# Kernel optimization log

Measured on AMD Instinct MI355X. Metric: run time of the kernel, lower is better.

Reference implementation:

```python
import jax, jax.numpy as jnp
import numpy as np

IOU_TR = 0.3
SCORE_TR = 0.1
EPS = 1e-9
N_DET = 4096
N_CLASSES = 20


def setup_inputs() -> dict:
    key = jax.random.key(0)
    k1, k2, k3, k4 = jax.random.split(key, 4)
    scores = jax.random.uniform(k1, (N_DET,), dtype=jnp.float32)
    classes = jax.random.randint(k2, (N_DET,), 0, N_CLASSES).astype(jnp.float32)
    centers = jax.random.uniform(k3, (N_DET, 3), dtype=jnp.float32) * 64.0
    dims = jax.random.uniform(k4, (N_DET, 3), dtype=jnp.float32) * 8.0 + 1.0
    results = jnp.concatenate([scores[:, None], classes[:, None], centers, dims], axis=1)
    return {"results": results}


def _pairwise_iou3d(boxes):
    # boxes: [N, 6] = (cx, cy, cz, w, h, d) center format
    c = boxes[:, :3]
    d = boxes[:, 3:]
    lo = c - d * 0.5  # [N,3]
    hi = c + d * 0.5
    inter_lo = jnp.maximum(lo[:, None, :], lo[None, :, :])  # [N,N,3]
    inter_hi = jnp.minimum(hi[:, None, :], hi[None, :, :])
    inter = jnp.prod(jnp.clip(inter_hi - inter_lo, 0.0, None), axis=-1)  # [N,N]
    vol = jnp.prod(d, axis=-1)  # [N]
    union = vol[:, None] + vol[None, :] - inter
    return inter / (union + EPS)


def reference(results):
    # results: [N, 8] = (score, class, cx, cy, cz, w, h, d)
    N = results.shape[0]
    order = jnp.argsort(-results[:, 0])  # sort by score descending
    r = results[order]
    valid = r[:, 0] >= SCORE_TR  # score threshold filter
    iou = _pairwise_iou3d(r[:, 2:])  # [N,N]
    idx = jnp.arange(N)

    def body(i, state):
        keep, active = state
        cur = active[i]
        keep = keep.at[i].set(cur)
        # suppress later boxes whose IoU with box i exceeds threshold
        sup = cur & (iou[i] > IOU_TR) & (idx > i)
        active = active & (~sup)
        return keep, active

    keep, _ = jax.lax.fori_loop(0, N, body, (jnp.zeros(N, dtype=bool), valid))
    # static-shape output: suppressed / filtered rows zeroed instead of compacted
    return jnp.where(keep[:, None], r, jnp.zeros_like(r))
```

## Files before the change

kernel.cpp:

```cpp
#include <hip/hip_runtime.h>

typedef unsigned long long u64;
typedef unsigned int u32;
typedef unsigned short u16;

#define N_DET 4096
#define NW 64
#define IOU_TR 0.3f
#define SCORE_TR 0.1f
#define EPS 1e-9f


__device__ __forceinline__ u64 rl64(u64 v, int l) {
    unsigned lo = __builtin_amdgcn_readlane((unsigned)v, l);
    unsigned hi = __builtin_amdgcn_readlane((unsigned)(v >> 32), l);
    return ((u64)hi << 32) | lo;
}

__global__ void __launch_bounds__(256) k_sort(const float* __restrict__ res,
                                              float* __restrict__ rows,
                                              float* __restrict__ ssc,
                                              float4* __restrict__ soaLO,
                                              float4* __restrict__ soaHI,
                                              u64* __restrict__ A,
                                              u64* __restrict__ Trm) {
    __shared__ float s[N_DET];
    int tid = threadIdx.x;
    if (blockIdx.x == 0) {
        if (tid < 64) A[tid] = 0ull;
        if (tid >= 64 && tid < 128)
            Trm[(size_t)4095 * NW + (tid - 64)] = 0ull;
    }
    for (int j = tid; j < N_DET; j += 256) s[j] = res[j * 8];
    __syncthreads();
    int r = tid >> 4, c = tid & 15;
    int gi = blockIdx.x * 16 + r;
    float sc = s[gi];
    int part = 0;
    int j0 = c * 256;
    for (int j = j0; j < j0 + 256; ++j) {
        float sj = s[j];
        part += (sj > sc) || (sj == sc && j < gi);
    }
    part += __shfl_xor(part, 1, 64);
    part += __shfl_xor(part, 2, 64);
    part += __shfl_xor(part, 4, 64);
    part += __shfl_xor(part, 8, 64);
    if (c == 0) {
        int rank = part;
        float4 a = *(const float4*)(res + gi * 8);
        float4 b = *(const float4*)(res + gi * 8 + 4);
        *(float4*)(rows + rank * 8)     = a;
        *(float4*)(rows + rank * 8 + 4) = b;
        ssc[rank] = a.x;
        float cx = a.z, cy = a.w, cz = b.x, dx = b.y, dy = b.z, dz = b.w;
        soaLO[rank] = make_float4(cx - dx * 0.5f, cy - dy * 0.5f,
                                  cz - dz * 0.5f, (dx * dy) * dz);
        soaHI[rank] = make_float4(cx + dx * 0.5f, cy + dy * 0.5f,
                                  cz + dz * 0.5f, 0.0f);
    }
}

__global__ void __launch_bounds__(256) k_sup(const float4* __restrict__ soaLO,
                                             const float4* __restrict__ soaHI,
                                             const float* __restrict__ ssc,
                                             u64* __restrict__ Trm,
                                             u64* __restrict__ A) {
    __shared__ float s_b[2][7][4][64];
    const int tid = threadIdx.x;
    const int wv = tid >> 6;
    const int lane = tid & 63;
    const int i0 = blockIdx.x * 4;
    const int i = i0 + wv;
    const int w0 = i0 >> 6;
    const bool valid = ssc[i] >= SCORE_TR;
    float4 iLO = soaLO[i];
    float4 iHI = soaHI[i];
    u64 rowword = 0, rowOr = 0;

    {
        int j = w0 * 64 + tid;
        int c = tid >> 6, l = tid & 63;
        if (j < N_DET) {
            float4 lo = soaLO[j], hi = soaHI[j];
            s_b[0][0][c][l] = lo.x; s_b[0][1][c][l] = lo.y;
            s_b[0][2][c][l] = lo.z; s_b[0][3][c][l] = lo.w;
            s_b[0][4][c][l] = hi.x; s_b[0][5][c][l] = hi.y;
            s_b[0][6][c][l] = hi.z;
        }
    }
    __syncthreads();

    for (int w = w0; w < NW; w += 4) {
        const int cur = ((w - w0) >> 2) & 1;
        const int jn = (w + 4) * 64 + tid;
        const bool inb = jn < N_DET;
        float4 nlo = make_float4(0.f, 0.f, 0.f, 0.f);
        float4 nhi = make_float4(0.f, 0.f, 0.f, 0.f);
        if (inb) { nlo = soaLO[jn]; nhi = soaHI[jn]; }

        const int nc = (NW - w < 4) ? (NW - w) : 4;
        for (int c = 0; c < nc; ++c) {
            int jj = (w + c) * 64 + lane;
            float lox = s_b[cur][0][c][lane], loy = s_b[cur][1][c][lane];
            float loz = s_b[cur][2][c][lane], vol = s_b[cur][3][c][lane];
            float hix = s_b[cur][4][c][lane], hiy = s_b[cur][5][c][lane];
            float hiz = s_b[cur][6][c][lane];
            float ix = fminf(iHI.x, hix) - fmaxf(iLO.x, lox); ix = fmaxf(ix, 0.f);
            float iy = fminf(iHI.y, hiy) - fmaxf(iLO.y, loy); iy = fmaxf(iy, 0.f);
            float iz = fminf(iHI.z, hiz) - fmaxf(iLO.z, loz); iz = fmaxf(iz, 0.f);
            float inter = (ix * iy) * iz;
            float uni = iLO.w + vol - inter;
            float iou = inter / (uni + EPS);
            u64 m = __ballot(iou > IOU_TR && jj > i);
            rowOr |= m;
            rowword = (lane == (w + c)) ? m : rowword;
        }
        if (inb) {
            int c = tid >> 6, l = tid & 63;
            s_b[cur ^ 1][0][c][l] = nlo.x; s_b[cur ^ 1][1][c][l] = nlo.y;
            s_b[cur ^ 1][2][c][l] = nlo.z; s_b[cur ^ 1][3][c][l] = nlo.w;
            s_b[cur ^ 1][4][c][l] = nhi.x; s_b[cur ^ 1][5][c][l] = nhi.y;
            s_b[cur ^ 1][6][c][l] = nhi.z;
        }
        __syncthreads();
    }

    if (valid && rowOr) {
        Trm[(size_t)i * NW + lane] = rowword;
        if (lane == 0) atomicOr(&A[i >> 6], 1ull << (i & 63));
    }
}

__global__ void __launch_bounds__(256, 1)
k_scan(const u64* __restrict__ Trm, const u64* __restrict__ A,
       const float* __restrict__ ssc, u64* __restrict__ keep) {
    __shared__ u64 s_valid[NW];
    __shared__ u16 s_nlist[4608];
    __shared__ int s_nsb;
    __shared__ u64 sbuf[2][48][64];
    const int tid = threadIdx.x;
    const int wv = tid >> 6;
    const int lane = tid & 63;

    for (int w = wv * 16; w < wv * 16 + 16; ++w) {
        float scw = ssc[w * 64 + lane];
        u64 m = __ballot(scw >= SCORE_TR);
        if (lane == 0) s_valid[w] = m;
    }
    __syncthreads();

    if (wv == 0) {
        u64 avA = A[lane] & s_valid[lane];
        int pc = __popcll(avA);
        int inc = pc;
#pragma unroll
        for (int d = 1; d < 64; d <<= 1) {
            int t = __shfl_up(inc, d, 64);
            if (lane >= d) inc += t;
        }
        int exc = inc - pc;
        int nTotal = __shfl(inc, 63, 64);
        u64 m = avA; int o = exc;
        while (m) {
            int k = __builtin_ctzll(m); m &= m - 1;
            s_nlist[o++] = (u16)(lane * 64 + k);
        }
        int nSB = (nTotal + 47) / 48;
        for (int t = nTotal + lane; t < (nSB + 1) * 48; t += 64)
            s_nlist[t] = (u16)4095;
        if (lane == 0) s_nsb = nSB;
    }
    __syncthreads();

    const int nSB = s_nsb;
    if (wv > 0 && nSB > 0) {
        const int base = (wv - 1) * 16;
#pragma unroll
        for (int s = 0; s < 16; ++s) {
            u32 si = (u32)s_nlist[base + s];
            sbuf[0][base + s][lane] = Trm[(size_t)si * NW + lane];
        }
    }
    u64 act = s_valid[lane];
    __syncthreads();

    for (int t = 0; t < nSB; ++t) {
        const int cur = t & 1;
        if (wv > 0) {
            const int base = (wv - 1) * 16;
            const int off = (t + 1) * 48 + base;
#pragma unroll
            for (int s = 0; s < 16; ++s) {
                u32 si = (u32)s_nlist[off + s];
                sbuf[cur ^ 1][base + s][lane] = Trm[(size_t)si * NW + lane];
            }
        } else {
            const int off = t * 48;
#pragma unroll
            for (int s = 0; s < 48; ++s) {
                u32 siv = (u32)s_nlist[off + s];
                u32 si = (u32)__builtin_amdgcn_readfirstlane((int)siv);
                u64 row = sbuf[cur][s][lane];
                u64 aw = rl64(act, (int)(si >> 6));
                u64 msk = 0ull - ((aw >> (si & 63u)) & 1ull);
                act &= ~(row & msk);
            }
        }
        __syncthreads();
    }
    if (wv == 0) keep[lane] = act;
}

__global__ void k_out(const float* __restrict__ rows,
                      const u64* __restrict__ keep,
                      float* __restrict__ out) {
    int i = blockIdx.x * 256 + threadIdx.x;
    bool kp = (keep[i >> 6] >> (i & 63)) & 1ull;
    float4 a = kp ? ((const float4*)rows)[i * 2]     : make_float4(0.f, 0.f, 0.f, 0.f);
    float4 b = kp ? ((const float4*)rows)[i * 2 + 1] : make_float4(0.f, 0.f, 0.f, 0.f);
    ((float4*)out)[i * 2]     = a;
    ((float4*)out)[i * 2 + 1] = b;
}

extern "C" void kernel_launch(void* const* d_in, const int* in_sizes, int n_in,
                              void* d_out, int out_size, void* d_ws, size_t ws_size,
                              hipStream_t stream) {
    const float* res = (const float*)d_in[0];
    float* out = (float*)d_out;

    float*  rows  = (float*)d_ws;
    float*  ssc   = rows + N_DET * 8;
    float4* soaLO = (float4*)(ssc + N_DET);
    float4* soaHI = soaLO + N_DET;
    u64*    A     = (u64*)(soaHI + N_DET);
    u64*    keep  = A + NW;
    u64*    Trm   = keep + NW;

    k_sort<<<N_DET / 16, 256, 0, stream>>>(res, rows, ssc, soaLO, soaHI, A, Trm);
    k_sup <<<N_DET / 4, 256, 0, stream>>>(soaLO, soaHI, ssc, Trm, A);
    k_scan<<<1, 256, 0, stream>>>(Trm, A, ssc, keep);
    k_out <<<16, 256, 0, stream>>>(rows, keep, out);
}
```

Baseline: 49.27 us.

## Batch suppression scan with speculative parallel apply and serial fallback on conflicts

Raises the super-block size in the single-block NMS scan from 48 to 96 rows. For each super-block, the active bits of all candidate rows are captured up front and their suppression masks are OR-ed together independently, which breaks the serial dependency chain. A check then tests whether any candidate in the batch is itself suppressed by that combined mask. If so, the exact serial loop reruns; otherwise the combined mask is applied at once. This shortens the critical path when conflicts are rare, at the cost of extra readlanes per batch and doubled shared-memory buffers.

```diff
diff --git a/kernel.cpp b/kernel.cpp
--- a/kernel.cpp
+++ b/kernel.cpp
@@ -9,6 +9,7 @@
 #define IOU_TR 0.3f
 #define SCORE_TR 0.1f
 #define EPS 1e-9f
+#define SB 96
 
 
 __device__ __forceinline__ u64 rl64(u64 v, int l) {
@@ -132,13 +133,15 @@
     }
 }
 
+#define KB(S) (((S) < 64) ? ((km0 >> (S)) & 1ull) : ((km1 >> ((S) - 64)) & 1ull))
+
 __global__ void __launch_bounds__(256, 1)
 k_scan(const u64* __restrict__ Trm, const u64* __restrict__ A,
        const float* __restrict__ ssc, u64* __restrict__ keep) {
     __shared__ u64 s_valid[NW];
-    __shared__ u16 s_nlist[4608];
+    __shared__ u16 s_nlist[4352];
     __shared__ int s_nsb;
-    __shared__ u64 sbuf[2][48][64];
+    __shared__ u64 sbuf[2][SB][64];
     const int tid = threadIdx.x;
     const int wv = tid >> 6;
     const int lane = tid & 63;
@@ -166,8 +169,8 @@
             int k = __builtin_ctzll(m); m &= m - 1;
             s_nlist[o++] = (u16)(lane * 64 + k);
         }
-        int nSB = (nTotal + 47) / 48;
-        for (int t = nTotal + lane; t < (nSB + 1) * 48; t += 64)
+        int nSB = (nTotal + SB - 1) / SB;
+        for (int t = nTotal + lane; t < (nSB + 1) * SB && t < 4352; t += 64)
             s_nlist[t] = (u16)4095;
         if (lane == 0) s_nsb = nSB;
     }
@@ -175,9 +178,9 @@
 
     const int nSB = s_nsb;
     if (wv > 0 && nSB > 0) {
-        const int base = (wv - 1) * 16;
-#pragma unroll
-        for (int s = 0; s < 16; ++s) {
+        const int base = (wv - 1) * 32;
+#pragma unroll
+        for (int s = 0; s < 32; ++s) {
             u32 si = (u32)s_nlist[base + s];
             sbuf[0][base + s][lane] = Trm[(size_t)si * NW + lane];
         }
@@ -188,23 +191,47 @@
     for (int t = 0; t < nSB; ++t) {
         const int cur = t & 1;
         if (wv > 0) {
-            const int base = (wv - 1) * 16;
-            const int off = (t + 1) * 48 + base;
-#pragma unroll
-            for (int s = 0; s < 16; ++s) {
+            const int base = (wv - 1) * 32;
+            const int off = (t + 1) * SB + base;
+#pragma unroll
+            for (int s = 0; s < 32; ++s) {
                 u32 si = (u32)s_nlist[off + s];
                 sbuf[cur ^ 1][base + s][lane] = Trm[(size_t)si * NW + lane];
             }
         } else {
-            const int off = t * 48;
-#pragma unroll
-            for (int s = 0; s < 48; ++s) {
-                u32 siv = (u32)s_nlist[off + s];
-                u32 si = (u32)__builtin_amdgcn_readfirstlane((int)siv);
-                u64 row = sbuf[cur][s][lane];
+            const int off = t * SB;
+            u64 km0 = 0ull, km1 = 0ull;
+#pragma unroll
+            for (int s = 0; s < SB; ++s) {
+                u32 si = (u32)s_nlist[off + s];
                 u64 aw = rl64(act, (int)(si >> 6));
-                u64 msk = 0ull - ((aw >> (si & 63u)) & 1ull);
-                act &= ~(row & msk);
+                u64 b = (aw >> (si & 63u)) & 1ull;
+                if (s < 64) km0 |= b << s; else km1 |= b << (s - 64);
+            }
+            u64 applied = 0ull;
+#pragma unroll
+            for (int s = 0; s < SB; ++s) {
+                u64 m_ = 0ull - KB(s);
+                applied |= sbuf[cur][s][lane] & m_;
+            }
+            u64 cfl = 0ull;
+#pragma unroll
+            for (int s = 0; s < SB; ++s) {
+                u32 si = (u32)s_nlist[off + s];
+                u64 ab = (rl64(applied, (int)(si >> 6)) >> (si & 63u)) & 1ull;
+                cfl |= ab & KB(s);
+            }
+            if (cfl) {
+                for (int s = 0; s < SB; ++s) {
+                    u32 siv = (u32)s_nlist[off + s];
+                    u32 si = (u32)__builtin_amdgcn_readfirstlane((int)siv);
+                    u64 row = sbuf[cur][s][lane];
+                    u64 aw = rl64(act, (int)(si >> 6));
+                    u64 msk = 0ull - ((aw >> (si & 63u)) & 1ull);
+                    act &= ~(row & msk);
+                }
+            } else {
+                act &= ~applied;
             }
         }
         __syncthreads();
```

Measured after the change: 71.77 us. 45.7% more time.
